# Optimization experiments

Measured on AMD Instinct MI355X. Metric: run time of the kernel, lower is better.

## Reference

```python
import jax, jax.numpy as jnp
from jax import lax
import numpy as np

EPS = 1e-5  # BatchNorm eps (inference mode; dropouts are identity in eval)


def _proj(img, w, g, b, m, v, stride):
    """All-heads Conv2d(3x3, no bias) + BatchNorm (inference) fused across heads.
    img: [B, Cin, H, W]; w: [heads, Cout, Cin, 3, 3]; g/b/m/v: [heads, Cout].
    Returns [B, heads, Cout, N'] (channels-first token layout)."""
    heads, Cout, Cin = w.shape[0], w.shape[1], w.shape[2]
    y = lax.conv_general_dilated(
        img, w.reshape(heads * Cout, Cin, 3, 3),
        window_strides=(stride, stride), padding=[(1, 1), (1, 1)],
        dimension_numbers=('NCHW', 'OIHW', 'NCHW'))
    B = y.shape[0]
    N = y.shape[2] * y.shape[3]
    y = y.reshape(B, heads, Cout, N)
    scale = g / jnp.sqrt(v + EPS)               # [heads, Cout]
    shift = b - m * scale
    return y * scale[None, :, :, None] + shift[None, :, :, None]


def reference(x, y, w_conv, bn_gamma, bn_beta, bn_mean, bn_var, w_out1, w_out2, h, w):
    B, N, C = x.shape
    xi = x.reshape(B, h, w, C).transpose(0, 3, 1, 2)  # b (h w) c -> b c h w
    yi = y.reshape(B, h, w, C).transpose(0, 3, 1, 2)
    scale_attn = C ** -0.5

    def P(i, img, stride):
        return _proj(img, w_conv[i], bn_gamma[i], bn_beta[i], bn_mean[i], bn_var[i], stride)

    # torch: query1(x), query2(y), key1(y), key2(x), value1(y), value2(x)
    Q1 = P(0, xi, 2)  # [B,h,C,Nq]
    Q2 = P(1, yi, 2)
    K1 = P(2, yi, 2)
    K2 = P(3, xi, 2)
    V1 = P(4, yi, 1)  # [B,h,C,Nv]
    V2 = P(5, xi, 1)

    # channel-attention: scores are [B, heads, C, C], softmax over last axis
    s1 = jnp.einsum('bhcn,bhdn->bhcd', Q2, K1) * scale_attn
    s2 = jnp.einsum('bhcn,bhdn->bhcd', Q1, K2) * scale_attn
    p1 = jax.nn.softmax(s1, axis=-1)
    p2 = jax.nn.softmax(s2, axis=-1)

    # context [B,heads,C,Nv] -> mean over heads -> [B,Nv,C]
    c1 = jnp.einsum('bhcd,bhdn->bhcn', p1, V1).mean(axis=1).transpose(0, 2, 1)
    c2 = jnp.einsum('bhcd,bhdn->bhcn', p2, V2).mean(axis=1).transpose(0, 2, 1)

    o1 = c1 @ w_out1.T  # Linear(dim_in, dim_out, bias=False)
    o2 = c2 @ w_out2.T
    return o1, o2


def setup_inputs() -> dict:
    B, C, HEADS, H, W = 8, 256, 4, 64, 64
    key = jax.random.key(0)
    ks = jax.random.split(key, 9)
    conv_std = 1.0 / np.sqrt(C * 9)
    lin_std = 1.0 / np.sqrt(C)
    return {
        'x': jax.random.normal(ks[0], (B, H * W, C), jnp.float32),
        'y': jax.random.normal(ks[1], (B, H * W, C), jnp.float32),
        'w_conv': jax.random.normal(ks[2], (6, HEADS, C, C, 3, 3), jnp.float32) * conv_std,
        'bn_gamma': jax.random.uniform(ks[3], (6, HEADS, C), jnp.float32, 0.5, 1.5),
        'bn_beta': jax.random.normal(ks[4], (6, HEADS, C), jnp.float32) * 0.1,
        'bn_mean': jax.random.normal(ks[5], (6, HEADS, C), jnp.float32) * 0.1,
        'bn_var': jax.random.uniform(ks[6], (6, HEADS, C), jnp.float32, 0.5, 1.5),
        'w_out1': jax.random.normal(ks[7], (C, C), jnp.float32) * lin_std,
        'w_out2': jax.random.normal(ks[8], (C, C), jnp.float32) * lin_std,
        'h': H,
        'w': W,
    }
```

## Files before the change

### kernel.cpp

```cpp
#include <hip/hip_runtime.h>
#include <stdint.h>

typedef __bf16 bf16_t;
typedef __bf16 bf16x8 __attribute__((ext_vector_type(8)));
typedef float f32x4 __attribute__((ext_vector_type(4)));

#define EPSBN 1e-5f

#define OFF_XP   ((size_t)0)
#define SZ_IMG   ((size_t)8*4356*256*2)
#define OFF_YP   (OFF_XP + SZ_IMG)
#define OFF_WQS  (OFF_YP + SZ_IMG)
#define SZ_WQS   ((size_t)4*1024*2304*2)
#define OFF_WVT  (OFF_WQS + SZ_WQS)
#define SZ_WVT   ((size_t)2*2304*1024*2)
#define OFF_W1B  (OFF_WVT + SZ_WVT)
#define SZ_WO    ((size_t)65536*2)
#define OFF_W2B  (OFF_W1B + SZ_WO)
#define OFF_SHQ  (OFF_W2B + SZ_WO)
#define SZ_SHQ   ((size_t)4096*4)
#define OFF_SHV  (OFF_SHQ + SZ_SHQ)
#define SZ_SHV   ((size_t)2048*4)
#define OFF_QK   (OFF_SHV + SZ_SHV)
#define SZ_QK    ((size_t)4*8*1024*1024*2)
#define OFF_S    (OFF_QK + SZ_QK)
#define SZ_S     ((size_t)2*8*4*65536*4)
#define OFF_PT   (OFF_S + SZ_S)
#define SZ_PT    ((size_t)2*8*4*65536*2)
#define OFF_A1   (OFF_PT + SZ_PT)
#define SZ_A1    ((size_t)2*8*256*1024*2)
#define OFF_WEFF (OFF_A1 + SZ_A1)
#define SZ_WEFF  ((size_t)2*8*256*2304*2)
#define OFF_BIAS (OFF_WEFF + SZ_WEFF)
#define SZ_BIAS  ((size_t)2*8*256*4)
#define WS_NEED  (OFF_BIAS + SZ_BIAS)

__device__ __forceinline__ void gload16(const bf16_t* g, bf16_t* l) {
  __builtin_amdgcn_global_load_lds(
      (const __attribute__((address_space(1))) void*)g,
      (__attribute__((address_space(3))) void*)l,
      16, 0, 0);
}

__device__ __forceinline__ int lb_off0() { return ((threadIdx.x >> 6)    ) * 512; }
__device__ __forceinline__ int lb_off1() { return ((threadIdx.x >> 6) + 4) * 512; }

template<int BSRC>
__device__ __forceinline__ void gemm_core(
    const bf16_t* __restrict__ A, int ldA,
    const bf16_t* __restrict__ B, int ldB,
    int m0, int n0, int KT, f32x4 acc[4][4])
{
  __shared__ bf16_t lA[2][4096];
  __shared__ bf16_t lB[2][4096];
  const int tid  = threadIdx.x;
  const int lane = tid & 63;
  const int wv   = tid >> 6;
  const int wr   = wv >> 1, wc = wv & 1;
  const int r4   = lane >> 2;
  const int k8   = (lane & 3) * 8;

  const bf16_t* gA0 = A + (size_t)(m0 + (wv    )*16 + r4) * ldA + k8;
  const bf16_t* gA1 = A + (size_t)(m0 + (wv + 4)*16 + r4) * ldA + k8;
  const int la0 = (wv    ) * 512;
  const int la1 = (wv + 4) * 512;
  const bf16_t* gB0 = B + (size_t)(n0 + (wv    )*16 + r4) * ldB + k8;
  const bf16_t* gB1 = B + (size_t)(n0 + (wv + 4)*16 + r4) * ldB + k8;
  (void)BSRC;

#pragma unroll
  for (int i = 0; i < 4; ++i)
#pragma unroll
    for (int j = 0; j < 4; ++j)
      acc[i][j] = f32x4{0.f, 0.f, 0.f, 0.f};

  const int lr = lane & 15;
  const int lk = (lane >> 4) * 8;
  int aidx[4], bidx[4];
#pragma unroll
  for (int f = 0; f < 4; ++f) {
    aidx[f] = (wr*64 + f*16 + lr)*32 + lk;
    bidx[f] = (wc*64 + f*16 + lr)*32 + lk;
  }

  auto stage = [&](int bufp, int kt) {
    const int kb = kt * 32;
    gload16(gA0 + kb, &lA[bufp][la0]);
    gload16(gA1 + kb, &lA[bufp][la1]);
    gload16(gB0 + kb, &lB[bufp][lb_off0()]);
    gload16(gB1 + kb, &lB[bufp][lb_off1()]);
  };

  stage(0, 0);
  __syncthreads();
  int buf = 0;
  for (int kt = 0; kt < KT; ++kt) {
    if (kt + 1 < KT) stage(buf ^ 1, kt + 1);
    bf16x8 av[4], bvv[4];
#pragma unroll
    for (int f = 0; f < 4; ++f) av[f]  = *(const bf16x8*)&lA[buf][aidx[f]];
#pragma unroll
    for (int f = 0; f < 4; ++f) bvv[f] = *(const bf16x8*)&lB[buf][bidx[f]];
#pragma unroll
    for (int i = 0; i < 4; ++i)
#pragma unroll
      for (int j = 0; j < 4; ++j)
        acc[i][j] = __builtin_amdgcn_mfma_f32_16x16x32_bf16(av[i], bvv[j], acc[i][j], 0, 0, 0);
    __syncthreads();
    buf ^= 1;
  }
}

template<int STRIDE>
__device__ __forceinline__ void conv256_core(
    const bf16_t* __restrict__ A, const bf16_t* __restrict__ img,
    int m0, int n0, f32x4 acc[8][4])
{
  __shared__ bf16_t lds[2][2][2][8192];
  const int tid  = threadIdx.x;
  const int lane = tid & 63;
  const int w    = tid >> 6;
  const int wm   = w >> 2;
  const int wn   = w & 3;

#pragma unroll
  for (int f = 0; f < 8; ++f)
#pragma unroll
    for (int j = 0; j < 4; ++j)
      acc[f][j] = f32x4{0.f, 0.f, 0.f, 0.f};

  const int srow = tid >> 2;
  const int ksX  = (tid & 3) ^ ((tid >> 3) & 3);
  const bf16_t* gA0 = A + (size_t)(m0 + srow      ) * 2304 + ksX*8;
  const bf16_t* gA1 = A + (size_t)(m0 + srow + 128) * 2304 + ksX*8;
  const int tk0 = n0 + srow, tk1 = tk0 + 128;
  int px0, px1;
  if (STRIDE == 1) { px0 = (tk0>>6)*66 + (tk0&63);      px1 = (tk1>>6)*66 + (tk1&63); }
  else             { px0 = ((tk0>>5)*2)*66 + (tk0&31)*2; px1 = ((tk1>>5)*2)*66 + (tk1&31)*2; }
  const bf16_t* gB0 = img + (size_t)px0*256 + ksX*8;
  const bf16_t* gB1 = img + (size_t)px1*256 + ksX*8;

  auto stageA = [&](int buf, int kh, int T) {
    const int kb = T*64 + kh*32;
    bf16_t* d = &lds[buf][0][kh][0] + tid*8;
    gload16(gA0 + kb, d);
    gload16(gA1 + kb, d + 4096);
  };
  auto stageB = [&](int buf, int kh, int T) {
    const int tap = T >> 2;
    const int ky  = (tap >= 6) ? 2 : ((tap >= 3) ? 1 : 0);
    const int kx  = tap - ky*3;
    const int ps  = (ky*66 + kx)*256 + (T & 3)*64 + kh*32;
    bf16_t* d = &lds[buf][1][kh][0] + tid*8;
    gload16(gB0 + ps, d);
    gload16(gB1 + ps, d + 4096);
  };

  const int lr    = lane & 15;
  const int slotS = (lane >> 4) ^ ((lane & 6) >> 1);
  int offA[8], offB[4];
#pragma unroll
  for (int f = 0; f < 8; ++f) offA[f] = (wm*128 + f*16 + lr)*32 + slotS*8;
#pragma unroll
  for (int nf = 0; nf < 4; ++nf) offB[nf] = (wn*64 + nf*16 + lr)*32 + slotS*8;

  stageA(0,0,0); stageB(0,0,0); stageA(0,1,0); stageB(0,1,0);
  stageA(1,0,1); stageB(1,0,1); stageA(1,1,1);
  __builtin_amdgcn_sched_barrier(0);
  asm volatile("s_waitcnt vmcnt(6)" ::: "memory");
  __builtin_amdgcn_sched_barrier(0);
  __builtin_amdgcn_s_barrier();
  __builtin_amdgcn_sched_barrier(0);

  const int NT = 36;
  for (int T = 0; T < NT; ++T) {
    const int buf = T & 1;
    const bool tail = (T >= NT - 2);
    bf16x8 av[8];
#pragma unroll
    for (int q = 0; q < 4; ++q) {
      const int kh = q >> 1;
      const int nh = q & 1;
      if (nh == 0) {
#pragma unroll
        for (int f = 0; f < 8; ++f)
          av[f] = *(const bf16x8*)(&lds[buf][0][kh][0] + offA[f]);
      }
      bf16x8 bv0 = *(const bf16x8*)(&lds[buf][1][kh][0] + offB[nh*2+0]);
      bf16x8 bv1 = *(const bf16x8*)(&lds[buf][1][kh][0] + offB[nh*2+1]);
      if      (q == 0) { if (T+1 < NT) stageB(buf^1, 1, T+1); }
      else if (q == 1) { if (T+2 < NT) stageA(buf,   0, T+2); }
      else if (q == 2) { if (T+2 < NT) stageB(buf,   0, T+2); }
      else             { if (T+2 < NT) stageA(buf,   1, T+2); }
      if (q == 2) {
        __builtin_amdgcn_sched_barrier(0);
        if (tail) asm volatile("s_waitcnt vmcnt(0)" ::: "memory");
        else      asm volatile("s_waitcnt vmcnt(4)" ::: "memory");
        __builtin_amdgcn_sched_barrier(0);
      }
      __builtin_amdgcn_s_barrier();
      asm volatile("s_waitcnt lgkmcnt(0)" ::: "memory");
      __builtin_amdgcn_sched_barrier(0);
      __builtin_amdgcn_s_setprio(1);
#pragma unroll
      for (int f = 0; f < 8; ++f) {
        acc[f][nh*2+0] = __builtin_amdgcn_mfma_f32_16x16x32_bf16(av[f], bv0, acc[f][nh*2+0], 0,0,0);
        acc[f][nh*2+1] = __builtin_amdgcn_mfma_f32_16x16x32_bf16(av[f], bv1, acc[f][nh*2+1], 0,0,0);
      }
      __builtin_amdgcn_s_setprio(0);
      __builtin_amdgcn_s_barrier();
      __builtin_amdgcn_sched_barrier(0);
    }
  }
}

__global__ __launch_bounds__(512) void k_conv_qk2(const bf16_t* __restrict__ wqs,
    const bf16_t* __restrict__ xp, const bf16_t* __restrict__ yp,
    bf16_t* __restrict__ qk, const float* __restrict__ shq)
{
  const int bx = blockIdx.x, b = blockIdx.y, ci = blockIdx.z;
  const int mt = bx >> 2, nt = bx & 3;
  const int m0 = mt*256, n0 = nt*256;
  const bf16_t* A = wqs + (size_t)ci * 1024 * 2304;
  const bf16_t* img = (((ci == 0) | (ci == 3)) ? xp : yp) + (size_t)b*4356*256;
  f32x4 acc[8][4];
  conv256_core<2>(A, img, m0, n0, acc);

  bf16_t* out = qk + (size_t)(ci*8 + b) * 1024 * 1024;
  const float* sh = shq + ci*1024;
  const int lane = threadIdx.x & 63, w = threadIdx.x >> 6;
  const int wm = w >> 2, wn = w & 3;
#pragma unroll
  for (int f = 0; f < 8; ++f) {
    const int row0 = m0 + wm*128 + f*16 + ((lane >> 4) << 2);
    const f32x4 s4 = *(const f32x4*)&sh[row0];
#pragma unroll
    for (int nf = 0; nf < 4; ++nf) {
      const int col = n0 + wn*64 + nf*16 + (lane & 15);
#pragma unroll
      for (int r = 0; r < 4; ++r)
        out[(size_t)(row0 + r)*1024 + col] = (bf16_t)(acc[f][nf][r] + s4[r]);
    }
  }
}

__global__ __launch_bounds__(512) void k_conv_out2(const bf16_t* __restrict__ weff,
    const bf16_t* __restrict__ xp, const bf16_t* __restrict__ yp,
    const float* __restrict__ bias, float* __restrict__ dout)
{
  const int nt = blockIdx.x, b = blockIdx.y, br = blockIdx.z;
  const int n0 = nt*256;
  const bf16_t* A = weff + (size_t)(br*8 + b)*589824;
  const bf16_t* img = ((br == 0) ? yp : xp) + (size_t)b*4356*256;
  f32x4 acc[8][4];
  conv256_core<1>(A, img, 0, n0, acc);

  float* outp = dout + (size_t)br*8388608 + (size_t)b*1048576;
  const float* bp = bias + (size_t)(br*8 + b)*256;
  const int lane = threadIdx.x & 63, w = threadIdx.x >> 6;
  const int wm = w >> 2, wn = w & 3;
#pragma unroll
  for (int f = 0; f < 8; ++f) {
    const int e0 = wm*128 + f*16 + ((lane >> 4) << 2);
    const f32x4 bv4 = *(const f32x4*)&bp[e0];
#pragma unroll
    for (int nf = 0; nf < 4; ++nf) {
      const int tok = n0 + wn*64 + nf*16 + (lane & 15);
      f32x4 v = acc[f][nf] + bv4;
      *(f32x4*)&outp[(size_t)tok*256 + e0] = v;
    }
  }
}

__global__ __launch_bounds__(256) void k_pack(const float* __restrict__ x, const float* __restrict__ y,
                                              bf16_t* __restrict__ xp, bf16_t* __restrict__ yp)
{
  const int p  = blockIdx.x;
  const int b  = blockIdx.y;
  const int im = blockIdx.z;
  const int c  = threadIdx.x;
  const int i = p / 66, j = p - i*66;
  const float* src = im ? y : x;
  bf16_t* dst = im ? yp : xp;
  float v = 0.f;
  if (i >= 1 && i <= 64 && j >= 1 && j <= 64)
    v = src[((size_t)b*4096 + (size_t)(i-1)*64 + (j-1))*256 + c];
  dst[((size_t)b*4356 + p)*256 + c] = (bf16_t)v;
}

__global__ __launch_bounds__(256) void k_prep_wq(const float* __restrict__ wcv,
    const float* __restrict__ g, const float* __restrict__ be,
    const float* __restrict__ mu, const float* __restrict__ va,
    bf16_t* __restrict__ wqs, float* __restrict__ shq)
{
  const int blk = blockIdx.x;
  __shared__ float lw[2304];
  const float* src = wcv + (size_t)blk * 2304;
  for (int t = threadIdx.x; t < 2304; t += 256) lw[t] = src[t];
  const float sc = g[blk] * rsqrtf(va[blk] + EPSBN);
  if (threadIdx.x == 0) shq[blk] = be[blk] - mu[blk]*sc;
  __syncthreads();
  bf16_t* dst = wqs + (size_t)blk * 2304;
  for (int t = threadIdx.x; t < 2304; t += 256) {
    const int tap = t >> 8, c = t & 255;
    dst[t] = (bf16_t)(lw[c*9 + tap] * sc);
  }
}

__global__ __launch_bounds__(256) void k_prep_wv(const float* __restrict__ wcv,
    const float* __restrict__ g, const float* __restrict__ va,
    bf16_t* __restrict__ wvT)
{
  const int cch = blockIdx.x;
  const int h = blockIdx.y >> 2, dc = blockIdx.y & 3;
  const int br = blockIdx.z;
  __shared__ float lw[64][72];
  __shared__ float lsc[64];
  const int ci = 4 + br;
  const int c0 = cch*8, d0 = dc*64;
  for (int e = threadIdx.x; e < 64*72; e += 256) {
    const int dd = e / 72, q = e - dd*72;
    lw[dd][q] = wcv[(size_t)(ci*1024 + h*256 + d0 + dd)*2304 + c0*9 + q];
  }
  if (threadIdx.x < 64) {
    const int bnIdx = ci*1024 + h*256 + d0 + threadIdx.x;
    lsc[threadIdx.x] = g[bnIdx] * rsqrtf(va[bnIdx] + EPSBN);
  }
  __syncthreads();
  for (int e = threadIdx.x; e < 72*64; e += 256) {
    const int kq = e >> 6, dd = e & 63;
    const int cc = kq / 9, tap = kq - cc*9;
    const int kp = tap*256 + c0 + cc;
    wvT[(size_t)br*2359296 + (size_t)kp*1024 + h*256 + d0 + dd] =
        (bf16_t)(lw[dd][cc*9 + tap] * lsc[dd]);
  }
}

__global__ __launch_bounds__(256) void k_small(const float* __restrict__ w1, const float* __restrict__ w2,
    const float* __restrict__ g, const float* __restrict__ be,
    const float* __restrict__ mu, const float* __restrict__ va,
    bf16_t* __restrict__ w1b, bf16_t* __restrict__ w2b, float* __restrict__ shv)
{
  const int idx = blockIdx.x*256 + threadIdx.x;
  if (idx < 65536) {
    w1b[idx] = (bf16_t)w1[idx];
  } else if (idx < 131072) {
    w2b[idx - 65536] = (bf16_t)w2[idx - 65536];
  } else if (idx < 133120) {
    const int t = idx - 131072;
    const int bnIdx = 4096 + t;
    const float sc = g[bnIdx] * rsqrtf(va[bnIdx] + EPSBN);
    shv[t] = be[bnIdx] - mu[bnIdx]*sc;
  }
}

__global__ __launch_bounds__(256) void k_gemm_s(const bf16_t* __restrict__ qk, float* __restrict__ sb)
{
  const int bx = blockIdx.x, by = blockIdx.y, br = blockIdx.z;
  const int mt = bx >> 1, nt = bx & 1;
  const int b = by >> 2, h = by & 3;
  const int ai = (br == 0) ? 1 : 0;
  const int bi = (br == 0) ? 2 : 3;
  const bf16_t* A  = qk + ((size_t)(ai*8 + b)*1024 + h*256) * 1024;
  const bf16_t* Bp = qk + ((size_t)(bi*8 + b)*1024 + h*256) * 1024;
  f32x4 acc[4][4];
  gemm_core<0>(A, 1024, Bp, 1024, mt*128, nt*128, 32, acc);

  float* out = sb + ((size_t)(br*8 + b)*4 + h) * 65536;
  const int lane = threadIdx.x & 63, wv = threadIdx.x >> 6;
  const int wr = wv >> 1, wc = wv & 1;
#pragma unroll
  for (int i = 0; i < 4; ++i) {
    const int row0 = mt*128 + wr*64 + i*16 + ((lane >> 4) << 2);
#pragma unroll
    for (int j = 0; j < 4; ++j) {
      const int col = nt*128 + wc*64 + j*16 + (lane & 15);
#pragma unroll
      for (int r = 0; r < 4; ++r)
        out[(size_t)(row0 + r)*256 + col] = acc[i][j][r];
    }
  }
}

__global__ __launch_bounds__(256) void k_softmax(const float* __restrict__ sb, bf16_t* __restrict__ pt)
{
  const int cc = blockIdx.x;
  const int bh = blockIdx.y;
  const int br = blockIdx.z;
  const size_t base = ((size_t)br*32 + bh) * 65536;
  __shared__ bf16_t lp[32][256];
  const int tid = threadIdx.x, lane = tid & 63, wv = tid >> 6;
  for (int r = 0; r < 8; ++r) {
    const int row = wv*8 + r;
    const float* srow = sb + base + (size_t)(cc*32 + row)*256;
    f32x4 v = ((const f32x4*)srow)[lane];
    v *= 0.0625f;
    float m = fmaxf(fmaxf(v[0], v[1]), fmaxf(v[2], v[3]));
#pragma unroll
    for (int o = 32; o; o >>= 1) m = fmaxf(m, __shfl_xor(m, o));
    const float e0 = __expf(v[0]-m), e1 = __expf(v[1]-m), e2 = __expf(v[2]-m), e3 = __expf(v[3]-m);
    float s = e0+e1+e2+e3;
#pragma unroll
    for (int o = 32; o; o >>= 1) s += __shfl_xor(s, o);
    const float inv = 0.25f / s;
    lp[row][lane*4+0] = (bf16_t)(e0*inv);
    lp[row][lane*4+1] = (bf16_t)(e1*inv);
    lp[row][lane*4+2] = (bf16_t)(e2*inv);
    lp[row][lane*4+3] = (bf16_t)(e3*inv);
  }
  __syncthreads();
  bf16_t* dst = pt + base;
  for (int it = 0; it < 32; ++it) {
    const int idx = it*256 + tid;
    const int d = idx >> 5, c = idx & 31;
    dst[(size_t)d*256 + cc*32 + c] = lp[c][d];
  }
}

__global__ __launch_bounds__(256) void k_gemm_a(const bf16_t* __restrict__ w1b, const bf16_t* __restrict__ w2b,
    const bf16_t* __restrict__ pt, bf16_t* __restrict__ a1)
{
  const int bx = blockIdx.x, by = blockIdx.y, br = blockIdx.z;
  const int mt = bx >> 1, nt = bx & 1;
  const int b = by >> 2, h = by & 3;
  const bf16_t* A  = br ? w2b : w1b;
  const bf16_t* Bp = pt + ((size_t)(br*8 + b)*4 + h) * 65536;
  f32x4 acc[4][4];
  gemm_core<0>(A, 256, Bp, 256, mt*128, nt*128, 8, acc);

  bf16_t* out = a1 + (size_t)(br*8 + b)*262144 + h*256;
  const int lane = threadIdx.x & 63, wv = threadIdx.x >> 6;
  const int wr = wv >> 1, wc = wv & 1;
#pragma unroll
  for (int i = 0; i < 4; ++i) {
    const int row0 = mt*128 + wr*64 + i*16 + ((lane >> 4) << 2);
#pragma unroll
    for (int j = 0; j < 4; ++j) {
      const int col = nt*128 + wc*64 + j*16 + (lane & 15);
#pragma unroll
      for (int r = 0; r < 4; ++r)
        out[(size_t)(row0 + r)*1024 + col] = (bf16_t)acc[i][j][r];
    }
  }
}

__global__ __launch_bounds__(256) void k_bias(const bf16_t* __restrict__ a1,
    const float* __restrict__ shv, float* __restrict__ bias)
{
  const int wv = threadIdx.x >> 6, lane = threadIdx.x & 63;
  const int e = blockIdx.x*4 + wv;
  const int b = blockIdx.y, br = blockIdx.z;
  const bf16_t* row = a1 + ((size_t)(br*8 + b)*256 + e)*1024;
  const float* sv = shv + br*1024;
  float acc = 0.f;
#pragma unroll
  for (int t = 0; t < 16; ++t) {
    const int idx = t*64 + lane;
    acc += (float)row[idx] * sv[idx];
  }
#pragma unroll
  for (int o = 32; o; o >>= 1) acc += __shfl_xor(acc, o);
  if (lane == 0) bias[(size_t)(br*8 + b)*256 + e] = acc;
}

__global__ __launch_bounds__(256) void k_gemm_weff(const bf16_t* __restrict__ a1,
    const bf16_t* __restrict__ wvT, bf16_t* __restrict__ weff)
{
  const int bx = blockIdx.x, b = blockIdx.y, br = blockIdx.z;
  const int mt = bx / 18, nt = bx - mt*18;
  const bf16_t* A  = a1 + (size_t)(br*8 + b)*262144;
  const bf16_t* Bp = wvT + (size_t)br*2359296;
  f32x4 acc[4][4];
  gemm_core<0>(A, 1024, Bp, 1024, mt*128, nt*128, 32, acc);

  bf16_t* out = weff + (size_t)(br*8 + b)*589824;
  const int lane = threadIdx.x & 63, wv = threadIdx.x >> 6;
  const int wr = wv >> 1, wc = wv & 1;
#pragma unroll
  for (int i = 0; i < 4; ++i) {
    const int row0 = mt*128 + wr*64 + i*16 + ((lane >> 4) << 2);
#pragma unroll
    for (int j = 0; j < 4; ++j) {
      const int col = nt*128 + wc*64 + j*16 + (lane & 15);
#pragma unroll
      for (int r = 0; r < 4; ++r)
        out[(size_t)(row0 + r)*2304 + col] = (bf16_t)acc[i][j][r];
    }
  }
}

extern "C" void kernel_launch(void* const* d_in, const int* in_sizes, int n_in,
                              void* d_out, int out_size, void* d_ws, size_t ws_size,
                              hipStream_t stream)
{
  (void)in_sizes; (void)n_in; (void)out_size;
  const float* x   = (const float*)d_in[0];
  const float* y   = (const float*)d_in[1];
  const float* wcv = (const float*)d_in[2];
  const float* bg  = (const float*)d_in[3];
  const float* bb  = (const float*)d_in[4];
  const float* bm  = (const float*)d_in[5];
  const float* bvv = (const float*)d_in[6];
  const float* w1  = (const float*)d_in[7];
  const float* w2  = (const float*)d_in[8];
  float* out = (float*)d_out;
  char* ws = (char*)d_ws;
  if (ws_size < WS_NEED) return;

  bf16_t* xp   = (bf16_t*)(ws + OFF_XP);
  bf16_t* yp   = (bf16_t*)(ws + OFF_YP);
  bf16_t* wqs  = (bf16_t*)(ws + OFF_WQS);
  bf16_t* wvT  = (bf16_t*)(ws + OFF_WVT);
  bf16_t* w1b  = (bf16_t*)(ws + OFF_W1B);
  bf16_t* w2b  = (bf16_t*)(ws + OFF_W2B);
  float*  shq  = (float*)(ws + OFF_SHQ);
  float*  shv  = (float*)(ws + OFF_SHV);
  bf16_t* qk   = (bf16_t*)(ws + OFF_QK);
  float*  sb   = (float*)(ws + OFF_S);
  bf16_t* pt   = (bf16_t*)(ws + OFF_PT);
  bf16_t* a1   = (bf16_t*)(ws + OFF_A1);
  bf16_t* weff = (bf16_t*)(ws + OFF_WEFF);
  float*  bias = (float*)(ws + OFF_BIAS);

  k_pack     <<<dim3(4356, 8, 2), 256, 0, stream>>>(x, y, xp, yp);
  k_prep_wq  <<<dim3(4096), 256, 0, stream>>>(wcv, bg, bb, bm, bvv, wqs, shq);
  k_prep_wv  <<<dim3(32, 16, 2), 256, 0, stream>>>(wcv, bg, bvv, wvT);
  k_small    <<<dim3(520), 256, 0, stream>>>(w1, w2, bg, bb, bm, bvv, w1b, w2b, shv);
  k_conv_qk2 <<<dim3(16, 8, 4), 512, 0, stream>>>(wqs, xp, yp, qk, shq);
  k_gemm_s   <<<dim3(4, 32, 2), 256, 0, stream>>>(qk, sb);
  k_softmax  <<<dim3(8, 32, 2), 256, 0, stream>>>(sb, pt);
  k_gemm_a   <<<dim3(4, 32, 2), 256, 0, stream>>>(w1b, w2b, pt, a1);
  k_bias     <<<dim3(64, 8, 2), 256, 0, stream>>>(a1, shv, bias);
  k_gemm_weff<<<dim3(36, 8, 2), 256, 0, stream>>>(a1, wvT, weff);
  k_conv_out2<<<dim3(16, 8, 2), 512, 0, stream>>>(weff, xp, yp, bias, out);
}
```

Baseline: 367.4 us.

## Restructure conv GEMM core into 4-stage LDS ring with register double-buffering

Replaces the two-buffer, quarter-step conv mainloop with a four-slot LDS ring of 32-wide K halves, prefetched three halves ahead. LDS fragments for the next half are loaded into a second register set while the current 32 MFMAs run, and the four barriers per 64-K step become one per half. Launch bounds now request two blocks per CU. This is meant to hide global and LDS latency and cut barrier overhead, at the cost of more VGPRs for the doubled fragment registers, which could cause spills under the tighter occupancy bound.

```diff
diff --git a/kernel.cpp b/kernel.cpp
--- a/kernel.cpp
+++ b/kernel.cpp
@@ -45,6 +45,8 @@
 __device__ __forceinline__ int lb_off0() { return ((threadIdx.x >> 6)    ) * 512; }
 __device__ __forceinline__ int lb_off1() { return ((threadIdx.x >> 6) + 4) * 512; }
 
+#define SBAR0 __builtin_amdgcn_sched_barrier(0)
+
 template<int BSRC>
 __device__ __forceinline__ void gemm_core(
     const bf16_t* __restrict__ A, int ldA,
@@ -116,7 +118,7 @@
     const bf16_t* __restrict__ A, const bf16_t* __restrict__ img,
     int m0, int n0, f32x4 acc[8][4])
 {
-  __shared__ bf16_t lds[2][2][2][8192];
+  __shared__ bf16_t lds[4][2][8192];
   const int tid  = threadIdx.x;
   const int lane = tid & 63;
   const int w    = tid >> 6;
@@ -131,90 +133,104 @@
 
   const int srow = tid >> 2;
   const int ksX  = (tid & 3) ^ ((tid >> 3) & 3);
-  const bf16_t* gA0 = A + (size_t)(m0 + srow      ) * 2304 + ksX*8;
-  const bf16_t* gA1 = A + (size_t)(m0 + srow + 128) * 2304 + ksX*8;
+  const bf16_t* gA0 = A + (size_t)(m0 + srow) * 2304 + ksX*8;
+  const bf16_t* gA1 = gA0 + (size_t)128 * 2304;
   const int tk0 = n0 + srow, tk1 = tk0 + 128;
   int px0, px1;
-  if (STRIDE == 1) { px0 = (tk0>>6)*66 + (tk0&63);      px1 = (tk1>>6)*66 + (tk1&63); }
+  if (STRIDE == 1) { px0 = (tk0>>6)*66 + (tk0&63);       px1 = (tk1>>6)*66 + (tk1&63); }
   else             { px0 = ((tk0>>5)*2)*66 + (tk0&31)*2; px1 = ((tk1>>5)*2)*66 + (tk1&31)*2; }
   const bf16_t* gB0 = img + (size_t)px0*256 + ksX*8;
   const bf16_t* gB1 = img + (size_t)px1*256 + ksX*8;
 
-  auto stageA = [&](int buf, int kh, int T) {
-    const int kb = T*64 + kh*32;
-    bf16_t* d = &lds[buf][0][kh][0] + tid*8;
-    gload16(gA0 + kb, d);
-    gload16(gA1 + kb, d + 4096);
-  };
-  auto stageB = [&](int buf, int kh, int T) {
+  auto stageHalf = [&](int half) {
+    const int s = half & 3;
+    bf16_t* dA = &lds[s][0][0] + tid*8;
+    gload16(gA0 + half*32, dA);
+    gload16(gA1 + half*32, dA + 4096);
+    const int T = half >> 1, kh = half & 1;
     const int tap = T >> 2;
     const int ky  = (tap >= 6) ? 2 : ((tap >= 3) ? 1 : 0);
     const int kx  = tap - ky*3;
     const int ps  = (ky*66 + kx)*256 + (T & 3)*64 + kh*32;
-    bf16_t* d = &lds[buf][1][kh][0] + tid*8;
-    gload16(gB0 + ps, d);
-    gload16(gB1 + ps, d + 4096);
+    bf16_t* dB = &lds[s][1][0] + tid*8;
+    gload16(gB0 + ps, dB);
+    gload16(gB1 + ps, dB + 4096);
   };
 
   const int lr    = lane & 15;
   const int slotS = (lane >> 4) ^ ((lane & 6) >> 1);
   int offA[8], offB[4];
 #pragma unroll
-  for (int f = 0; f < 8; ++f) offA[f] = (wm*128 + f*16 + lr)*32 + slotS*8;
-#pragma unroll
-  for (int nf = 0; nf < 4; ++nf) offB[nf] = (wn*64 + nf*16 + lr)*32 + slotS*8;
-
-  stageA(0,0,0); stageB(0,0,0); stageA(0,1,0); stageB(0,1,0);
-  stageA(1,0,1); stageB(1,0,1); stageA(1,1,1);
-  __builtin_amdgcn_sched_barrier(0);
-  asm volatile("s_waitcnt vmcnt(6)" ::: "memory");
-  __builtin_amdgcn_sched_barrier(0);
+  for (int f = 0; f < 8; ++f)  offA[f] = (wm*128 + f*16 + lr)*32 + slotS*8;
+#pragma unroll
+  for (int n = 0; n < 4; ++n)  offB[n] = (wn*64  + n*16 + lr)*32 + slotS*8;
+
+#define LOADREGS(HALF, AV, BV) do {                                        \
+    const int s_ = (HALF) & 3;                                             \
+    const bf16_t* pA_ = &lds[s_][0][0];                                    \
+    const bf16_t* pB_ = &lds[s_][1][0];                                    \
+    _Pragma("unroll") for (int f_ = 0; f_ < 8; ++f_)                       \
+      AV[f_] = *(const bf16x8*)(pA_ + offA[f_]);                           \
+    _Pragma("unroll") for (int n_ = 0; n_ < 4; ++n_)                       \
+      BV[n_] = *(const bf16x8*)(pB_ + offB[n_]);                           \
+  } while (0)
+
+#define MFMA32(AV, BV) do {                                                \
+    __builtin_amdgcn_s_setprio(1);                                         \
+    _Pragma("unroll") for (int f_ = 0; f_ < 8; ++f_)                       \
+      _Pragma("unroll") for (int n_ = 0; n_ < 4; ++n_)                     \
+        acc[f_][n_] = __builtin_amdgcn_mfma_f32_16x16x32_bf16(             \
+            AV[f_], BV[n_], acc[f_][n_], 0, 0, 0);                         \
+    __builtin_amdgcn_s_setprio(0);                                         \
+  } while (0)
+
+  stageHalf(0); stageHalf(1); stageHalf(2);
+  SBAR0;
+  asm volatile("s_waitcnt vmcnt(4)" ::: "memory");
+  SBAR0;
   __builtin_amdgcn_s_barrier();
-  __builtin_amdgcn_sched_barrier(0);
-
-  const int NT = 36;
-  for (int T = 0; T < NT; ++T) {
-    const int buf = T & 1;
-    const bool tail = (T >= NT - 2);
-    bf16x8 av[8];
-#pragma unroll
-    for (int q = 0; q < 4; ++q) {
-      const int kh = q >> 1;
-      const int nh = q & 1;
-      if (nh == 0) {
-#pragma unroll
-        for (int f = 0; f < 8; ++f)
-          av[f] = *(const bf16x8*)(&lds[buf][0][kh][0] + offA[f]);
-      }
-      bf16x8 bv0 = *(const bf16x8*)(&lds[buf][1][kh][0] + offB[nh*2+0]);
-      bf16x8 bv1 = *(const bf16x8*)(&lds[buf][1][kh][0] + offB[nh*2+1]);
-      if      (q == 0) { if (T+1 < NT) stageB(buf^1, 1, T+1); }
-      else if (q == 1) { if (T+2 < NT) stageA(buf,   0, T+2); }
-      else if (q == 2) { if (T+2 < NT) stageB(buf,   0, T+2); }
-      else             { if (T+2 < NT) stageA(buf,   1, T+2); }
-      if (q == 2) {
-        __builtin_amdgcn_sched_barrier(0);
-        if (tail) asm volatile("s_waitcnt vmcnt(0)" ::: "memory");
-        else      asm volatile("s_waitcnt vmcnt(4)" ::: "memory");
-        __builtin_amdgcn_sched_barrier(0);
-      }
-      __builtin_amdgcn_s_barrier();
+  SBAR0;
+
+  bf16x8 avP[8], bvP[4], avN[8], bvN[4];
+  LOADREGS(0, avP, bvP);
+
+  for (int h = 0; h < 72; h += 2) {
+    if (h + 3 < 72) stageHalf(h + 3);
+    LOADREGS(h + 1, avN, bvN);
+    SBAR0;
+    if (h < 69) { asm volatile("s_waitcnt vmcnt(4)" ::: "memory"); }
+    else        { asm volatile("s_waitcnt vmcnt(0)" ::: "memory"); }
+    SBAR0;
+    asm volatile("s_waitcnt lgkmcnt(12)" ::: "memory");
+    SBAR0;
+    MFMA32(avP, bvP);
+    __builtin_amdgcn_s_barrier();
+    SBAR0;
+
+    const int h1 = h + 1;
+    if (h1 + 3 < 72) stageHalf(h1 + 3);
+    if (h1 < 71) {
+      LOADREGS(h1 + 1, avP, bvP);
+      SBAR0;
+      if (h1 < 69) { asm volatile("s_waitcnt vmcnt(4)" ::: "memory"); }
+      else         { asm volatile("s_waitcnt vmcnt(0)" ::: "memory"); }
+      SBAR0;
+      asm volatile("s_waitcnt lgkmcnt(12)" ::: "memory");
+      SBAR0;
+    } else {
+      SBAR0;
       asm volatile("s_waitcnt lgkmcnt(0)" ::: "memory");
-      __builtin_amdgcn_sched_barrier(0);
-      __builtin_amdgcn_s_setprio(1);
-#pragma unroll
-      for (int f = 0; f < 8; ++f) {
-        acc[f][nh*2+0] = __builtin_amdgcn_mfma_f32_16x16x32_bf16(av[f], bv0, acc[f][nh*2+0], 0,0,0);
-        acc[f][nh*2+1] = __builtin_amdgcn_mfma_f32_16x16x32_bf16(av[f], bv1, acc[f][nh*2+1], 0,0,0);
-      }
-      __builtin_amdgcn_s_setprio(0);
-      __builtin_amdgcn_s_barrier();
-      __builtin_amdgcn_sched_barrier(0);
+      SBAR0;
     }
-  }
-}
-
-__global__ __launch_bounds__(512) void k_conv_qk2(const bf16_t* __restrict__ wqs,
+    MFMA32(avN, bvN);
+    __builtin_amdgcn_s_barrier();
+    SBAR0;
+  }
+#undef LOADREGS
+#undef MFMA32
+}
+
+__global__ __launch_bounds__(512, 2) void k_conv_qk2(const bf16_t* __restrict__ wqs,
     const bf16_t* __restrict__ xp, const bf16_t* __restrict__ yp,
     bf16_t* __restrict__ qk, const float* __restrict__ shq)
 {
@@ -244,7 +260,7 @@
   }
 }
 
-__global__ __launch_bounds__(512) void k_conv_out2(const bf16_t* __restrict__ weff,
+__global__ __launch_bounds__(512, 2) void k_conv_out2(const bf16_t* __restrict__ weff,
     const bf16_t* __restrict__ xp, const bf16_t* __restrict__ yp,
     const float* __restrict__ bias, float* __restrict__ dout)
 {
```

Result: no change. 368.4 us (+0.3%).
